# Kernel optimization log

Measured on AMD Instinct MI355X. Metric: run time of the kernel, lower is better.

## Reference

```python
import jax, jax.numpy as jnp
import numpy as np

N = 50000   # num nodes
E = 600000  # num edges (avg degree 12)
IN = 128
OUT = 128


def setup_inputs() -> dict:
    key = jax.random.key(0)
    ks = jax.random.split(key, 6)
    x = jax.random.normal(ks[0], (N, IN), dtype=jnp.float32)
    edge_index = jax.random.randint(ks[1], (2, E), 0, N, dtype=jnp.int32)
    # glorot-ish scaling for the linear weights
    W1 = jax.random.normal(ks[2], (IN, OUT), dtype=jnp.float32) / np.float32(np.sqrt(IN))
    b1 = jnp.zeros((OUT,), dtype=jnp.float32)
    W2 = jax.random.normal(ks[3], (OUT, OUT), dtype=jnp.float32) / np.float32(np.sqrt(OUT))
    b2 = jnp.zeros((OUT,), dtype=jnp.float32)
    return {"x": x, "edge_index": edge_index, "W1": W1, "b1": b1, "W2": W2, "b2": b2}


def gcn_conv(x, src, dst, W, b):
    # PyG GCNConv defaults: add self-loops, symmetric normalization D^-1/2 A D^-1/2.
    n = x.shape[0]
    deg = jax.ops.segment_sum(jnp.ones_like(dst, dtype=x.dtype), dst, num_segments=n)
    dinv = jnp.where(deg > 0, jax.lax.rsqrt(deg), 0.0)
    norm = dinv[src] * dinv[dst]            # [E+N]
    h = x @ W                               # [N, OUT]
    msg = h[src] * norm[:, None]            # gather + scale
    out = jax.ops.segment_sum(msg, dst, num_segments=n)  # scatter-add
    return out + b


def reference(x, edge_index, W1, b1, W2, b2):
    loop = jnp.arange(N, dtype=edge_index.dtype)
    src = jnp.concatenate([edge_index[0], loop])  # self-loops appended
    dst = jnp.concatenate([edge_index[1], loop])
    h = jax.nn.relu(gcn_conv(x, src, dst, W1, b1))
    out = jax.nn.relu(gcn_conv(h, src, dst, W2, b2))
    return out
```

## Files before the change

### kernel.cpp

```cpp
#include <hip/hip_runtime.h>
#include <hip/hip_bf16.h>


#define CAP 64

typedef short s16x8 __attribute__((ext_vector_type(8)));
typedef float f32x4 __attribute__((ext_vector_type(4)));

__device__ __forceinline__ unsigned short bf16_rne(float f) {
    unsigned u = __float_as_uint(f);
    return (unsigned short)((u + 0x7fffu + ((u >> 16) & 1u)) >> 16);
}


__global__ void setup_k(const float* __restrict__ W1, const float* __restrict__ W2,
                        short* __restrict__ wh1, short* __restrict__ wl1,
                        short* __restrict__ wh2, short* __restrict__ wl2,
                        int* __restrict__ cursor, int n) {
    int b = blockIdx.x;
    if (b >= 128) {
        int i = (b - 128) * 1024 + threadIdx.x * 4;
        if (i < n) {
            int4 z = make_int4(0, 0, 0, 0);
            if (i + 4 <= n) *(int4*)(cursor + i) = z;
            else for (int j = i; j < n; ++j) cursor[j] = 0;
        }
        return;
    }
    int gid = b * 256 + threadIdx.x;
    int which = gid >> 14;
    int tid = gid & 16383;
    const float* W = which ? W2 : W1;
    short* wh = which ? wh2 : wh1;
    short* wl = which ? wl2 : wl1;
    int k = tid >> 7, nn = tid & 127;
    float w = W[tid];
    unsigned u = __float_as_uint(w);
    unsigned hibits = (u + 0x7fffu + ((u >> 16) & 1u)) & 0xffff0000u;
    float rem = w - __uint_as_float(hibits);
    int kt = k >> 5, kr = k & 31, nt = nn >> 4, nr = nn & 15;
    int l = ((kr >> 3) << 4) | nr;
    int j = kr & 7;
    int dest = ((kt * 8 + nt) * 64 + l) * 8 + j;
    wh[dest] = (short)(hibits >> 16);
    wl[dest] = (short)bf16_rne(rem);
}

__global__ void fill_k(const int* __restrict__ src, const int* __restrict__ dst,
                       int* __restrict__ cursor, int* __restrict__ adj, int E) {
    int e = blockIdx.x * 256 + threadIdx.x;
    if (e < E) {
        int d = dst[e];
        int p = atomicAdd(&cursor[d], 1);
        if (p < CAP) adj[(size_t)d * CAP + p] = src[e];
    }
}

__device__ __forceinline__ void gemm_tile_compute(const char* lds,
                                                  const s16x8 BH[4][2], const s16x8 BL[4][2],
                                                  const int* __restrict__ cursor,
                                                  unsigned short* __restrict__ Hb,
                                                  int base, int n, int w, int rl, int kg) {
#pragma unroll
    for (int rt = 0; rt < 4; ++rt) {
        int row_local = rt * 16 + rl;
        int arow_byte = row_local * 256;
        int aswz = (row_local & 7) << 4;
        f32x4 acc[2] = {(f32x4){0.f,0.f,0.f,0.f}, (f32x4){0.f,0.f,0.f,0.f}};
#pragma unroll
        for (int kt = 0; kt < 4; ++kt) {
            int coff = (kt * 64 + (kg << 4)) ^ aswz;
            s16x8 ah = *(const s16x8*)(lds + arow_byte + coff);
            s16x8 al = *(const s16x8*)(lds + 16384 + arow_byte + coff);
#pragma unroll
            for (int i = 0; i < 2; ++i) {
                acc[i] = __builtin_amdgcn_mfma_f32_16x16x32_bf16(ah, BH[kt][i], acc[i], 0, 0, 0);
                acc[i] = __builtin_amdgcn_mfma_f32_16x16x32_bf16(al, BH[kt][i], acc[i], 0, 0, 0);
                acc[i] = __builtin_amdgcn_mfma_f32_16x16x32_bf16(ah, BL[kt][i], acc[i], 0, 0, 0);
            }
        }
        int r0 = base + rt * 16 + (kg << 2);
        float d0 = (r0 + 0 < n) ? rsqrtf((float)(cursor[r0 + 0] + 1)) : 0.f;
        float d1 = (r0 + 1 < n) ? rsqrtf((float)(cursor[r0 + 1] + 1)) : 0.f;
        float d2 = (r0 + 2 < n) ? rsqrtf((float)(cursor[r0 + 2] + 1)) : 0.f;
        float d3 = (r0 + 3 < n) ? rsqrtf((float)(cursor[r0 + 3] + 1)) : 0.f;
#pragma unroll
        for (int i = 0; i < 2; ++i) {
            int col = ((w * 2 + i) << 4) | rl;
            if (r0 + 0 < n) Hb[(size_t)(r0 + 0) * 128 + col] = bf16_rne(acc[i][0] * d0);
            if (r0 + 1 < n) Hb[(size_t)(r0 + 1) * 128 + col] = bf16_rne(acc[i][1] * d1);
            if (r0 + 2 < n) Hb[(size_t)(r0 + 2) * 128 + col] = bf16_rne(acc[i][2] * d2);
            if (r0 + 3 < n) Hb[(size_t)(r0 + 3) * 128 + col] = bf16_rne(acc[i][3] * d3);
        }
    }
}

__global__ __launch_bounds__(256) void gemm_mfma_f32(const float* __restrict__ X,
                                                     const short* __restrict__ wbh,
                                                     const short* __restrict__ wbl,
                                                     const int* __restrict__ cursor,
                                                     unsigned short* __restrict__ Hb,
                                                     int n) {
    __shared__ char lds[32768];
    int tid = threadIdx.x;
    int w = tid >> 6;
    int l = tid & 63;
    int rl = l & 15;
    int kg = l >> 4;
    int base = blockIdx.x * 64;

    const s16x8* bh8 = (const s16x8*)wbh;
    const s16x8* bl8 = (const s16x8*)wbl;
    s16x8 BH[4][2], BL[4][2];
#pragma unroll
    for (int kt = 0; kt < 4; ++kt)
#pragma unroll
        for (int i = 0; i < 2; ++i) {
            int f = kt * 8 + (w * 2 + i);
            BH[kt][i] = bh8[f * 64 + l];
            BL[kt][i] = bl8[f * 64 + l];
        }

#pragma unroll
    for (int u = 0; u < 4; ++u) {
        int idx = u * 256 + tid;
        int r = idx >> 4;
        int c0 = (idx & 15) * 8;
        int row = base + r;
        float v[8];
        if (row < n) {
            const float4* p = (const float4*)(X + (size_t)row * 128 + c0);
            float4 a = p[0], b = p[1];
            v[0]=a.x; v[1]=a.y; v[2]=a.z; v[3]=a.w;
            v[4]=b.x; v[5]=b.y; v[6]=b.z; v[7]=b.w;
        } else {
#pragma unroll
            for (int i = 0; i < 8; ++i) v[i] = 0.f;
        }
        short hi8[8], lo8[8];
#pragma unroll
        for (int i = 0; i < 8; ++i) {
            unsigned uu = __float_as_uint(v[i]);
            unsigned hb = (uu + 0x7fffu + ((uu >> 16) & 1u)) & 0xffff0000u;
            float rem = v[i] - __uint_as_float(hb);
            hi8[i] = (short)(hb >> 16);
            lo8[i] = (short)bf16_rne(rem);
        }
        int boff = r * 256 + ((c0 * 2) ^ ((r & 7) << 4));
        *(s16x8*)(lds + boff)         = *(const s16x8*)hi8;
        *(s16x8*)(lds + 16384 + boff) = *(const s16x8*)lo8;
    }
    __syncthreads();
    gemm_tile_compute(lds, BH, BL, cursor, Hb, base, n, w, rl, kg);
}

__global__ __launch_bounds__(256) void gemm_mfma_bf16(const unsigned short* __restrict__ XH,
                                                      const unsigned short* __restrict__ XL,
                                                      const short* __restrict__ wbh,
                                                      const short* __restrict__ wbl,
                                                      const int* __restrict__ cursor,
                                                      unsigned short* __restrict__ Hb,
                                                      int n) {
    __shared__ char lds[32768];
    int tid = threadIdx.x;
    int w = tid >> 6;
    int l = tid & 63;
    int rl = l & 15;
    int kg = l >> 4;
    int base = blockIdx.x * 64;

    const s16x8* bh8 = (const s16x8*)wbh;
    const s16x8* bl8 = (const s16x8*)wbl;
    s16x8 BH[4][2], BL[4][2];
#pragma unroll
    for (int kt = 0; kt < 4; ++kt)
#pragma unroll
        for (int i = 0; i < 2; ++i) {
            int f = kt * 8 + (w * 2 + i);
            BH[kt][i] = bh8[f * 64 + l];
            BL[kt][i] = bl8[f * 64 + l];
        }

#pragma unroll
    for (int u = 0; u < 8; ++u) {
        int idx = u * 256 + tid;
        int plane = idx >> 10;
        int ci = idx & 1023;
        int r = ci >> 4;
        int cb = (ci & 15) * 16;
        int row = base + r;
        const unsigned short* src = plane ? XL : XH;
        s16x8 val = {0,0,0,0,0,0,0,0};
        if (row < n) val = *(const s16x8*)(src + (size_t)row * 128 + cb / 2);
        int boff = plane * 16384 + r * 256 + (cb ^ ((r & 7) << 4));
        *(s16x8*)(lds + boff) = val;
    }
    __syncthreads();
    gemm_tile_compute(lds, BH, BL, cursor, Hb, base, n, w, rl, kg);
}


template <int SPLIT>
__global__ __launch_bounds__(256) void agg_k(const unsigned short* __restrict__ Hs,
                                             const int* __restrict__ cursor,
                                             const int* __restrict__ adj,
                                             const float* __restrict__ bias,
                                             float* __restrict__ fout,
                                             unsigned short* __restrict__ th,
                                             unsigned short* __restrict__ tl,
                                             int n) {
    int node = blockIdx.x * 4 + (threadIdx.x >> 6);
    if (node >= n) return;
    node = __builtin_amdgcn_readfirstlane(node);
    int lane = threadIdx.x & 63;

    const unsigned* H1 = (const unsigned*)Hs;
    unsigned sraw = H1[(size_t)node * 64 + lane];
    float ax = __uint_as_float((sraw & 0xffffu) << 16);
    float ay = __uint_as_float(sraw & 0xffff0000u);

    int deg_raw = cursor[node];
    int e1 = deg_raw > CAP ? CAP : deg_raw;
    const int* alist = adj + (size_t)node * CAP;
    int e = 0;

    for (; e + 16 <= e1; e += 16) {
        int s[16];
#pragma unroll
        for (int i = 0; i < 16; ++i) s[i] = alist[e + i];
        unsigned rv[16];
#pragma unroll
        for (int i = 0; i < 16; ++i) rv[i] = H1[(size_t)s[i] * 64 + lane];
#pragma unroll
        for (int i = 0; i < 16; ++i) {
            ax += __uint_as_float((rv[i] & 0xffffu) << 16);
            ay += __uint_as_float(rv[i] & 0xffff0000u);
        }
    }
    for (; e + 4 <= e1; e += 4) {
        int s[4];
#pragma unroll
        for (int i = 0; i < 4; ++i) s[i] = alist[e + i];
        unsigned rv[4];
#pragma unroll
        for (int i = 0; i < 4; ++i) rv[i] = H1[(size_t)s[i] * 64 + lane];
#pragma unroll
        for (int i = 0; i < 4; ++i) {
            ax += __uint_as_float((rv[i] & 0xffffu) << 16);
            ay += __uint_as_float(rv[i] & 0xffff0000u);
        }
    }
    for (; e < e1; ++e) {
        unsigned rv = H1[(size_t)alist[e] * 64 + lane];
        ax += __uint_as_float((rv & 0xffffu) << 16);
        ay += __uint_as_float(rv & 0xffff0000u);
    }

    float di = rsqrtf((float)(deg_raw + 1));
    float2 b = ((const float2*)bias)[lane];
    float a0 = fmaxf(fmaf(ax, di, b.x), 0.f);
    float a1 = fmaxf(fmaf(ay, di, b.y), 0.f);
    if (SPLIT) {
        unsigned short h0 = bf16_rne(a0), h1 = bf16_rne(a1);
        float r0 = a0 - __uint_as_float(((unsigned)h0) << 16);
        float r1 = a1 - __uint_as_float(((unsigned)h1) << 16);
        ((ushort2*)th)[(size_t)node * 64 + lane] = make_ushort2(h0, h1);
        ((ushort2*)tl)[(size_t)node * 64 + lane] = make_ushort2(bf16_rne(r0), bf16_rne(r1));
    } else {
        ((float2*)fout)[(size_t)node * 64 + lane] = make_float2(a0, a1);
    }
}


extern "C" void kernel_launch(void* const* d_in, const int* in_sizes, int n_in,
                              void* d_out, int out_size, void* d_ws, size_t ws_size,
                              hipStream_t stream) {
    const float* x  = (const float*)d_in[0];
    const int*   ei = (const int*)d_in[1];
    const float* W1 = (const float*)d_in[2];
    const float* b1 = (const float*)d_in[3];
    const float* W2 = (const float*)d_in[4];
    const float* b2 = (const float*)d_in[5];
    float* out = (float*)d_out;

    const int N = in_sizes[0] / 128;
    const int E = in_sizes[1] / 2;
    const int* src = ei;
    const int* dst = ei + E;

    char* ws = (char*)d_ws;
    size_t off = 0;
    auto alloc = [&](size_t bytes) -> void* {
        void* p = ws + off;
        off = (off + bytes + 255) & ~(size_t)255;
        return p;
    };
    int*   cursor  = (int*)  alloc((size_t)N * 4);
    int*   adj     = (int*)  alloc((size_t)N * CAP * 4);
    unsigned short* hb = (unsigned short*)alloc((size_t)N * 128 * 2);
    unsigned short* th = (unsigned short*)alloc((size_t)N * 128 * 2);
    unsigned short* tl = (unsigned short*)alloc((size_t)N * 128 * 2);
    short* w1h = (short*)alloc((size_t)128 * 128 * 2);
    short* w1l = (short*)alloc((size_t)128 * 128 * 2);
    short* w2h = (short*)alloc((size_t)128 * 128 * 2);
    short* w2l = (short*)alloc((size_t)128 * 128 * 2);
    (void)ws_size; (void)n_in; (void)out_size;

    int gE = (E + 255) / 256;
    int gA = (N + 3) / 4;
    int gG = (N + 63) / 64;
    int zb = (N + 1023) / 1024;

    setup_k<<<128 + zb, 256, 0, stream>>>(W1, W2, w1h, w1l, w2h, w2l, cursor, N);
    fill_k<<<gE, 256, 0, stream>>>(src, dst, cursor, adj, E);

    gemm_mfma_f32<<<gG, 256, 0, stream>>>(x, w1h, w1l, cursor, hb, N);
    agg_k<1><<<gA, 256, 0, stream>>>(hb, cursor, adj, b1, nullptr, th, tl, N);
    gemm_mfma_bf16<<<gG, 256, 0, stream>>>(th, tl, w2h, w2l, cursor, hb, N);
    agg_k<0><<<gA, 256, 0, stream>>>(hb, cursor, adj, b2, out, nullptr, nullptr, N);
}
```

Before: 125.3 us.

## Fuse layer-1 aggregation into layer-2 GEMM tile via LDS

Replaces the separate layer-1 aggregation kernel and bf16 GEMM with one kernel where each block aggregates its 64 nodes' neighbor features, splits them into hi/lo bf16, writes them into swizzled LDS, then runs the MFMA tile. This removes the global write and re-read of the split intermediate and one kernel launch. In exchange each wave gathers 16 nodes sequentially with far fewer waves in flight, which may reduce latency hiding for the irregular gathers.

```diff
diff --git a/kernel.cpp b/kernel.cpp
--- a/kernel.cpp
+++ b/kernel.cpp
@@ -154,19 +154,19 @@
     gemm_tile_compute(lds, BH, BL, cursor, Hb, base, n, w, rl, kg);
 }
 
-__global__ __launch_bounds__(256) void gemm_mfma_bf16(const unsigned short* __restrict__ XH,
-                                                      const unsigned short* __restrict__ XL,
-                                                      const short* __restrict__ wbh,
-                                                      const short* __restrict__ wbl,
-                                                      const int* __restrict__ cursor,
-                                                      unsigned short* __restrict__ Hb,
-                                                      int n) {
+
+__global__ __launch_bounds__(256) void agg_gemm_k(const unsigned short* __restrict__ Hs,
+                                                  const int* __restrict__ cursor,
+                                                  const int* __restrict__ adj,
+                                                  const float* __restrict__ bias,
+                                                  const short* __restrict__ wbh,
+                                                  const short* __restrict__ wbl,
+                                                  unsigned short* __restrict__ Hb2,
+                                                  int n) {
     __shared__ char lds[32768];
     int tid = threadIdx.x;
     int w = tid >> 6;
     int l = tid & 63;
-    int rl = l & 15;
-    int kg = l >> 4;
     int base = blockIdx.x * 64;
 
     const s16x8* bh8 = (const s16x8*)wbh;
@@ -181,34 +181,81 @@
             BL[kt][i] = bl8[f * 64 + l];
         }
 
-#pragma unroll
-    for (int u = 0; u < 8; ++u) {
-        int idx = u * 256 + tid;
-        int plane = idx >> 10;
-        int ci = idx & 1023;
-        int r = ci >> 4;
-        int cb = (ci & 15) * 16;
-        int row = base + r;
-        const unsigned short* src = plane ? XL : XH;
-        s16x8 val = {0,0,0,0,0,0,0,0};
-        if (row < n) val = *(const s16x8*)(src + (size_t)row * 128 + cb / 2);
-        int boff = plane * 16384 + r * 256 + (cb ^ ((r & 7) << 4));
-        *(s16x8*)(lds + boff) = val;
+    const unsigned* H1 = (const unsigned*)Hs;
+    float2 b = ((const float2*)bias)[l];
+
+    for (int i = 0; i < 16; ++i) {
+        int row = w * 16 + i;
+        int node = base + row;
+        unsigned hiw = 0, low = 0;
+        if (node < n) {
+            int nd = __builtin_amdgcn_readfirstlane(node);
+            unsigned sraw = H1[(size_t)nd * 64 + l];
+            float ax = __uint_as_float((sraw & 0xffffu) << 16);
+            float ay = __uint_as_float(sraw & 0xffff0000u);
+
+            int deg_raw = cursor[nd];
+            int e1 = deg_raw > CAP ? CAP : deg_raw;
+            const int* alist = adj + (size_t)nd * CAP;
+            int e = 0;
+            for (; e + 16 <= e1; e += 16) {
+                int s[16];
+#pragma unroll
+                for (int j = 0; j < 16; ++j) s[j] = alist[e + j];
+                unsigned rv[16];
+#pragma unroll
+                for (int j = 0; j < 16; ++j) rv[j] = H1[(size_t)s[j] * 64 + l];
+#pragma unroll
+                for (int j = 0; j < 16; ++j) {
+                    ax += __uint_as_float((rv[j] & 0xffffu) << 16);
+                    ay += __uint_as_float(rv[j] & 0xffff0000u);
+                }
+            }
+            for (; e + 4 <= e1; e += 4) {
+                int s[4];
+#pragma unroll
+                for (int j = 0; j < 4; ++j) s[j] = alist[e + j];
+                unsigned rv[4];
+#pragma unroll
+                for (int j = 0; j < 4; ++j) rv[j] = H1[(size_t)s[j] * 64 + l];
+#pragma unroll
+                for (int j = 0; j < 4; ++j) {
+                    ax += __uint_as_float((rv[j] & 0xffffu) << 16);
+                    ay += __uint_as_float(rv[j] & 0xffff0000u);
+                }
+            }
+            for (; e < e1; ++e) {
+                unsigned rv = H1[(size_t)alist[e] * 64 + l];
+                ax += __uint_as_float((rv & 0xffffu) << 16);
+                ay += __uint_as_float(rv & 0xffff0000u);
+            }
+
+            float di = rsqrtf((float)(deg_raw + 1));
+            float a0 = fmaxf(fmaf(ax, di, b.x), 0.f);
+            float a1 = fmaxf(fmaf(ay, di, b.y), 0.f);
+            unsigned short h0 = bf16_rne(a0), h1 = bf16_rne(a1);
+            float r0 = a0 - __uint_as_float(((unsigned)h0) << 16);
+            float r1 = a1 - __uint_as_float(((unsigned)h1) << 16);
+            hiw = (unsigned)h0 | ((unsigned)h1 << 16);
+            low = (unsigned)bf16_rne(r0) | ((unsigned)bf16_rne(r1) << 16);
+        }
+        int boff = row * 256 + ((l * 4) ^ ((row & 7) << 4));
+        *(unsigned*)(lds + boff)         = hiw;
+        *(unsigned*)(lds + 16384 + boff) = low;
     }
     __syncthreads();
-    gemm_tile_compute(lds, BH, BL, cursor, Hb, base, n, w, rl, kg);
-}
-
-
-template <int SPLIT>
+
+    int rl = l & 15;
+    int kg = l >> 4;
+    gemm_tile_compute(lds, BH, BL, cursor, Hb2, base, n, w, rl, kg);
+}
+
+
 __global__ __launch_bounds__(256) void agg_k(const unsigned short* __restrict__ Hs,
                                              const int* __restrict__ cursor,
                                              const int* __restrict__ adj,
                                              const float* __restrict__ bias,
-                                             float* __restrict__ fout,
-                                             unsigned short* __restrict__ th,
-                                             unsigned short* __restrict__ tl,
-                                             int n) {
+                                             float* __restrict__ fout, int n) {
     int node = blockIdx.x * 4 + (threadIdx.x >> 6);
     if (node >= n) return;
     node = __builtin_amdgcn_readfirstlane(node);
@@ -260,15 +307,7 @@
     float2 b = ((const float2*)bias)[lane];
     float a0 = fmaxf(fmaf(ax, di, b.x), 0.f);
     float a1 = fmaxf(fmaf(ay, di, b.y), 0.f);
-    if (SPLIT) {
-        unsigned short h0 = bf16_rne(a0), h1 = bf16_rne(a1);
-        float r0 = a0 - __uint_as_float(((unsigned)h0) << 16);
-        float r1 = a1 - __uint_as_float(((unsigned)h1) << 16);
-        ((ushort2*)th)[(size_t)node * 64 + lane] = make_ushort2(h0, h1);
-        ((ushort2*)tl)[(size_t)node * 64 + lane] = make_ushort2(bf16_rne(r0), bf16_rne(r1));
-    } else {
-        ((float2*)fout)[(size_t)node * 64 + lane] = make_float2(a0, a1);
-    }
+    ((float2*)fout)[(size_t)node * 64 + lane] = make_float2(a0, a1);
 }
 
 
@@ -297,9 +336,8 @@
     };
     int*   cursor  = (int*)  alloc((size_t)N * 4);
     int*   adj     = (int*)  alloc((size_t)N * CAP * 4);
-    unsigned short* hb = (unsigned short*)alloc((size_t)N * 128 * 2);
-    unsigned short* th = (unsigned short*)alloc((size_t)N * 128 * 2);
-    unsigned short* tl = (unsigned short*)alloc((size_t)N * 128 * 2);
+    unsigned short* hb  = (unsigned short*)alloc((size_t)N * 128 * 2);
+    unsigned short* hb2 = (unsigned short*)alloc((size_t)N * 128 * 2);
     short* w1h = (short*)alloc((size_t)128 * 128 * 2);
     short* w1l = (short*)alloc((size_t)128 * 128 * 2);
     short* w2h = (short*)alloc((size_t)128 * 128 * 2);
@@ -315,7 +353,6 @@
     fill_k<<<gE, 256, 0, stream>>>(src, dst, cursor, adj, E);
 
     gemm_mfma_f32<<<gG, 256, 0, stream>>>(x, w1h, w1l, cursor, hb, N);
-    agg_k<1><<<gA, 256, 0, stream>>>(hb, cursor, adj, b1, nullptr, th, tl, N);
-    gemm_mfma_bf16<<<gG, 256, 0, stream>>>(th, tl, w2h, w2l, cursor, hb, N);
-    agg_k<0><<<gA, 256, 0, stream>>>(hb, cursor, adj, b2, out, nullptr, nullptr, N);
-}
+    agg_gemm_k<<<gG, 256, 0, stream>>>(hb, cursor, adj, b1, w2h, w2l, hb2, N);
+    agg_k<<<gA, 256, 0, stream>>>(hb2, cursor, adj, b2, out, N);
+}
```

Measured after the change: 161.0 us. 28.5% more time.
